# Optimization experiments

Measured on AMD Instinct MI355X. Metric: run time of the kernel, lower is better.

Reference implementation:

```python
import jax, jax.numpy as jnp
import numpy as np

B = 128
N_ATOMS = 4096
NB, NA, NT = 4095, 4094, 4093
MAX_LEN = 5 * NT  # 20465, longest packed column (torsions)
EPS = 1e-8


def setup_inputs() -> dict:
    key = jax.random.key(0)
    ks = jax.random.split(key, 24)
    feats = jnp.zeros((B, MAX_LEN, 9), jnp.float32)
    # col 0: atom type ids
    atoms = jax.random.randint(ks[0], (B, N_ATOMS), 0, 6)
    # col 5: coords, flattened (N_ATOMS, 3)
    coords = jax.random.normal(ks[1], (B, N_ATOMS, 3), jnp.float32) * 5.0
    # col 6: bonds (i, j, type)
    bonds = jnp.stack([
        jax.random.randint(ks[2], (B, NB), 0, N_ATOMS),
        jax.random.randint(ks[3], (B, NB), 0, N_ATOMS),
        jax.random.randint(ks[4], (B, NB), 0, 15)], axis=-1)
    # col 7: angles (i, j, k, type)
    angles = jnp.stack([
        jax.random.randint(ks[5], (B, NA), 0, N_ATOMS),
        jax.random.randint(ks[6], (B, NA), 0, N_ATOMS),
        jax.random.randint(ks[7], (B, NA), 0, N_ATOMS),
        jax.random.randint(ks[8], (B, NA), 0, 13)], axis=-1)
    # col 8: torsions (i, j, k, l, type)
    tors = jnp.stack([
        jax.random.randint(ks[9], (B, NT), 0, N_ATOMS),
        jax.random.randint(ks[10], (B, NT), 0, N_ATOMS),
        jax.random.randint(ks[11], (B, NT), 0, N_ATOMS),
        jax.random.randint(ks[12], (B, NT), 0, N_ATOMS),
        jax.random.randint(ks[13], (B, NT), 0, 25)], axis=-1)
    feats = feats.at[:, :N_ATOMS, 0].set(atoms.astype(jnp.float32))
    feats = feats.at[:, :3 * N_ATOMS, 5].set(coords.reshape(B, -1))
    feats = feats.at[:, :3 * NB, 6].set(bonds.reshape(B, -1).astype(jnp.float32))
    feats = feats.at[:, :4 * NA, 7].set(angles.reshape(B, -1).astype(jnp.float32))
    feats = feats.at[:, :5 * NT, 8].set(tors.reshape(B, -1).astype(jnp.float32))
    lengths = jnp.tile(jnp.array(
        [[N_ATOMS, 0, 0, 0, 0, 3 * N_ATOMS, 3 * NB, 4 * NA, 5 * NT]],
        jnp.int32), (B, 1))
    bond_type = jnp.stack([jnp.ones(15), jax.random.uniform(ks[14], (15,), minval=1.0, maxval=2.0)], -1).astype(jnp.float32)
    angle_type = jnp.stack([jnp.ones(13), jax.random.uniform(ks[15], (13,), minval=1.0, maxval=3.0)], -1).astype(jnp.float32)
    tor_type = jnp.stack([jnp.ones(25), jax.random.uniform(ks[16], (25,), minval=0.0, maxval=3.14)], -1).astype(jnp.float32)
    multiplicity = jax.random.randint(ks[17], (25,), 1, 4)
    opt_pars = jax.random.uniform(ks[18], (47,), minval=0.5, maxval=1.5).astype(jnp.float32)
    return {"features": feats, "lengths": lengths, "bond_type": bond_type,
            "angle_type": angle_type, "tor_type": tor_type,
            "multiplicity": multiplicity, "opt_pars": opt_pars}


def _sample_energy(f, bond_type, angle_type, tor_type, multiplicity, opt_pars):
    coords = f[:3 * N_ATOMS, 5].reshape(-1, 3)                      # [N,3]
    bonds = f[:3 * NB, 6].astype(jnp.int32).reshape(-1, 3)          # [NB,3]
    angles = f[:4 * NA, 7].astype(jnp.int32).reshape(-1, 4)         # [NA,4]
    tors = f[:5 * NT, 8].astype(jnp.int32).reshape(-1, 5)           # [NT,5]

    # bonds: harmonic k*(r - r0)^2
    d = coords[bonds[:, 0]] - coords[bonds[:, 1]]
    r = jnp.sqrt(jnp.sum(d * d, -1) + EPS)
    pb = bond_type[bonds[:, 2]]
    e_bond = opt_pars[0] * jnp.sum(pb[:, 0] * (r - pb[:, 1]) ** 2)

    # angles: harmonic k*(theta - theta0)^2
    v1 = coords[angles[:, 0]] - coords[angles[:, 1]]
    v2 = coords[angles[:, 2]] - coords[angles[:, 1]]
    cosang = jnp.sum(v1 * v2, -1) / (
        jnp.sqrt(jnp.sum(v1 * v1, -1) + EPS) * jnp.sqrt(jnp.sum(v2 * v2, -1) + EPS))
    theta = jnp.arccos(jnp.clip(cosang, -1.0 + 1e-6, 1.0 - 1e-6))
    pa = angle_type[angles[:, 3]]
    e_ang = opt_pars[1] * jnp.sum(pa[:, 0] * (theta - pa[:, 1]) ** 2)

    # torsions: periodic k*(1 + cos(n*phi - delta))
    ci, cj, ck, cl = (coords[tors[:, m]] for m in range(4))
    b1, b2, b3 = cj - ci, ck - cj, cl - ck
    n1 = jnp.cross(b1, b2)
    n2 = jnp.cross(b2, b3)
    b2n = b2 / jnp.sqrt(jnp.sum(b2 * b2, -1, keepdims=True) + EPS)
    m1 = jnp.cross(n1, b2n)
    phi = jnp.arctan2(jnp.sum(m1 * n2, -1), jnp.sum(n1 * n2, -1))
    pt = tor_type[tors[:, 4]]
    n_mult = multiplicity[tors[:, 4]].astype(jnp.float32)
    e_tor = opt_pars[2] * jnp.sum(pt[:, 0] * (1.0 + jnp.cos(n_mult * phi - pt[:, 1])))

    return jnp.stack([e_bond, e_ang, e_tor])


def reference(features, lengths, bond_type, angle_type, tor_type, multiplicity, opt_pars):
    # lengths are uniform across batch (constants above); vmap over batch dim
    return jax.vmap(_sample_energy, in_axes=(0, None, None, None, None, None))(
        features, bond_type, angle_type, tor_type, multiplicity, opt_pars)
```

## Files before the change

kernel.cpp:

```cpp
#include <hip/hip_runtime.h>
#include <math.h>

#define BATCH    128
#define N_ATOMS  4096
#define NB       4095
#define NA       4094
#define NT       4093
#define FSTRIDE  184185
#define ROWS     20465
#define CROWS    12288
#define BROWS    12285
#define AROWS    16376
#define EPSV     1e-8f
#define THREADS  1024
#define WAVES    16
#define TPR      120

typedef float float4a __attribute__((ext_vector_type(4), aligned(4)));

__global__ __launch_bounds__(THREADS, 1) void
local_energy_v11(const float* __restrict__ F,
                 const float* __restrict__ bond_type,
                 const float* __restrict__ angle_type,
                 const float* __restrict__ tor_type,
                 const int*   __restrict__ multiplicity,
                 const float* __restrict__ opt_pars,
                 float*       __restrict__ out)
{
    __shared__ float          scc[CROWS];
    __shared__ unsigned short sbB[BROWS + 1];
    __shared__ unsigned short sbA[AROWS];
    __shared__ unsigned short sbT[ROWS + 1];
    __shared__ float sbt[30], sat[26], stt[50], smu[25];
    __shared__ float sred[WAVES * 2];

    const int b   = blockIdx.x;
    const int x   = b & 7;
    const int g   = b >> 3;
    const int s   = (g & 15) * 8 + x;
    const int p   = g >> 4;
    const int tid = threadIdx.x;
    const int w   = tid >> 6;
    const int l   = tid & 63;
    const size_t sbase = (size_t)s * FSTRIDE;

    if (tid < 30)                      sbt[tid]       = bond_type[tid];
    else if (tid >= 32 && tid < 58)    sat[tid - 32]  = angle_type[tid - 32];
    else if (tid >= 64 && tid < 114)   stt[tid - 64]  = tor_type[tid - 64];
    else if (tid >= 128 && tid < 153)  smu[tid - 128] = (float)multiplicity[tid - 128];

    const int tmax = p ? 137 : 171;
    for (int t = w; t < tmax; t += WAVES) {
        const int R0 = TPR * t + 2 * l;
        const int R1 = R0 + 1;
        float4a v0, v1;
        const bool ok0 = (R0 < ROWS);
        const bool ok1 = (R1 < ROWS);
        if (ok0) v0 = *(const float4a*)(F + sbase + (size_t)9 * R0 + 5);
        if (ok1) v1 = *(const float4a*)(F + sbase + (size_t)9 * R1 + 5);

        if (R1 < CROWS) {
            float2 c2; c2.x = v0.x; c2.y = v1.x;
            *(float2*)(scc + R0) = c2;
        }
        if (p) {
            if (R1 < BROWS) {
                unsigned pk = (unsigned)(unsigned short)(int)v0.y
                            | ((unsigned)(unsigned short)(int)v1.y << 16);
                *(unsigned*)(sbB + R0) = pk;
            } else if (R0 < BROWS) {
                sbB[R0] = (unsigned short)(int)v0.y;
            }
            if (R1 < AROWS) {
                unsigned pk = (unsigned)(unsigned short)(int)v0.z
                            | ((unsigned)(unsigned short)(int)v1.z << 16);
                *(unsigned*)(sbA + R0) = pk;
            }
        } else {
            if (ok1) {
                unsigned pk = (unsigned)(unsigned short)(int)v0.w
                            | ((unsigned)(unsigned short)(int)v1.w << 16);
                *(unsigned*)(sbT + R0) = pk;
            } else if (ok0) {
                sbT[R0] = (unsigned short)(int)v0.w;
            }
        }
    }
    __syncthreads();

    float eA = 0.f, eB = 0.f;
    if (p) {
        for (int i = tid; i < NB; i += THREADS) {
            const int a0 = sbB[3 * i + 0];
            const int a1 = sbB[3 * i + 1];
            const int bt = sbB[3 * i + 2];
            const float dx = scc[3 * a0 + 0] - scc[3 * a1 + 0];
            const float dy = scc[3 * a0 + 1] - scc[3 * a1 + 1];
            const float dz = scc[3 * a0 + 2] - scc[3 * a1 + 2];
            const float r  = sqrtf(dx * dx + dy * dy + dz * dz + EPSV);
            const float t0 = r - sbt[bt * 2 + 1];
            eA += sbt[bt * 2 + 0] * t0 * t0;
        }
        for (int i = tid; i < NA; i += THREADS) {
            const int a0 = sbA[4 * i + 0];
            const int a1 = sbA[4 * i + 1];
            const int a2 = sbA[4 * i + 2];
            const int at = sbA[4 * i + 3];
            const float v1x = scc[3 * a0 + 0] - scc[3 * a1 + 0];
            const float v1y = scc[3 * a0 + 1] - scc[3 * a1 + 1];
            const float v1z = scc[3 * a0 + 2] - scc[3 * a1 + 2];
            const float v2x = scc[3 * a2 + 0] - scc[3 * a1 + 0];
            const float v2y = scc[3 * a2 + 1] - scc[3 * a1 + 1];
            const float v2z = scc[3 * a2 + 2] - scc[3 * a1 + 2];
            const float d12 = v1x * v2x + v1y * v2y + v1z * v2z;
            const float n1  = sqrtf(v1x * v1x + v1y * v1y + v1z * v1z + EPSV);
            const float n2  = sqrtf(v2x * v2x + v2y * v2y + v2z * v2z + EPSV);
            float cosang = d12 / (n1 * n2);
            cosang = fminf(fmaxf(cosang, -1.0f + 1e-6f), 1.0f - 1e-6f);
            const float t0 = acosf(cosang) - sat[at * 2 + 1];
            eB += sat[at * 2 + 0] * t0 * t0;
        }
    } else {
        for (int i = tid; i < NT; i += THREADS) {
            const int ai = sbT[5 * i + 0];
            const int aj = sbT[5 * i + 1];
            const int ak = sbT[5 * i + 2];
            const int al = sbT[5 * i + 3];
            const int tt = sbT[5 * i + 4];
            const float b1x = scc[3*aj+0] - scc[3*ai+0];
            const float b1y = scc[3*aj+1] - scc[3*ai+1];
            const float b1z = scc[3*aj+2] - scc[3*ai+2];
            const float b2x = scc[3*ak+0] - scc[3*aj+0];
            const float b2y = scc[3*ak+1] - scc[3*aj+1];
            const float b2z = scc[3*ak+2] - scc[3*aj+2];
            const float b3x = scc[3*al+0] - scc[3*ak+0];
            const float b3y = scc[3*al+1] - scc[3*ak+1];
            const float b3z = scc[3*al+2] - scc[3*ak+2];
            const float n1x = b1y*b2z - b1z*b2y;
            const float n1y = b1z*b2x - b1x*b2z;
            const float n1z = b1x*b2y - b1y*b2x;
            const float n2x = b2y*b3z - b2z*b3y;
            const float n2y = b2z*b3x - b2x*b3z;
            const float n2z = b2x*b3y - b2y*b3x;
            const float inv = 1.0f / sqrtf(b2x*b2x + b2y*b2y + b2z*b2z + EPSV);
            const float bnx = b2x * inv, bny = b2y * inv, bnz = b2z * inv;
            const float m1x = n1y*bnz - n1z*bny;
            const float m1y = n1z*bnx - n1x*bnz;
            const float m1z = n1x*bny - n1y*bnx;
            const float phi = atan2f(m1x*n2x + m1y*n2y + m1z*n2z,
                                     n1x*n2x + n1y*n2y + n1z*n2z);
            eA += stt[tt * 2 + 0] * (1.0f + cosf(smu[tt] * phi - stt[tt * 2 + 1]));
        }
    }

    for (int off = 32; off > 0; off >>= 1) {
        eA += __shfl_down(eA, off);
        eB += __shfl_down(eB, off);
    }
    if (l == 0) {
        sred[w * 2 + 0] = eA;
        sred[w * 2 + 1] = eB;
    }
    __syncthreads();
    if (tid == 0) {
        float rA = 0.f, rB = 0.f;
        for (int i = 0; i < WAVES; ++i) { rA += sred[i * 2]; rB += sred[i * 2 + 1]; }
        if (p) {
            out[s * 3 + 0] = opt_pars[0] * rA;
            out[s * 3 + 1] = opt_pars[1] * rB;
        } else {
            out[s * 3 + 2] = opt_pars[2] * rA;
        }
    }
}

extern "C" void kernel_launch(void* const* d_in, const int* in_sizes, int n_in,
                              void* d_out, int out_size, void* d_ws, size_t ws_size,
                              hipStream_t stream) {
    const float* F            = (const float*)d_in[0];
    const float* bond_type    = (const float*)d_in[2];
    const float* angle_type   = (const float*)d_in[3];
    const float* tor_type     = (const float*)d_in[4];
    const int*   multiplicity = (const int*)  d_in[5];
    const float* opt_pars     = (const float*)d_in[6];
    float* out = (float*)d_out;

    local_energy_v11<<<dim3(BATCH * 2), dim3(THREADS), 0, stream>>>(
        F, bond_type, angle_type, tor_type, multiplicity, opt_pars, out);
}
```

Baseline: 154.1 us.

## Merge bond/angle and torsion blocks into one block per sample

Replaces the two-blocks-per-sample split, where one block did bonds and angles and the other did torsions, with a single 1024-thread block per sample that computes all three energies. Each sample's feature rows are then staged into shared memory once instead of twice, removing redundant global reads of the coordinate column. The staging loop is also unrolled by two so each wave issues four vector loads before any shared-memory stores. The trade-off is half as many blocks (128 versus 256) and longer serial work per block, which can leave many compute units idle on a large GPU.

```diff
diff --git a/kernel.cpp b/kernel.cpp
--- a/kernel.cpp
+++ b/kernel.cpp
@@ -15,11 +15,13 @@
 #define THREADS  1024
 #define WAVES    16
 #define TPR      120
+#define NTILES   171
 
 typedef float float4a __attribute__((ext_vector_type(4), aligned(4)));
 
+
 __global__ __launch_bounds__(THREADS, 1) void
-local_energy_v11(const float* __restrict__ F,
+local_energy_v12(const float* __restrict__ F,
                  const float* __restrict__ bond_type,
                  const float* __restrict__ angle_type,
                  const float* __restrict__ tor_type,
@@ -32,13 +34,9 @@
     __shared__ unsigned short sbA[AROWS];
     __shared__ unsigned short sbT[ROWS + 1];
     __shared__ float sbt[30], sat[26], stt[50], smu[25];
-    __shared__ float sred[WAVES * 2];
-
-    const int b   = blockIdx.x;
-    const int x   = b & 7;
-    const int g   = b >> 3;
-    const int s   = (g & 15) * 8 + x;
-    const int p   = g >> 4;
+    __shared__ float sred[WAVES * 3];
+
+    const int s   = blockIdx.x;
     const int tid = threadIdx.x;
     const int w   = tid >> 6;
     const int l   = tid & 63;
@@ -49,128 +47,160 @@
     else if (tid >= 64 && tid < 114)   stt[tid - 64]  = tor_type[tid - 64];
     else if (tid >= 128 && tid < 153)  smu[tid - 128] = (float)multiplicity[tid - 128];
 
-    const int tmax = p ? 137 : 171;
-    for (int t = w; t < tmax; t += WAVES) {
-        const int R0 = TPR * t + 2 * l;
-        const int R1 = R0 + 1;
-        float4a v0, v1;
-        const bool ok0 = (R0 < ROWS);
-        const bool ok1 = (R1 < ROWS);
-        if (ok0) v0 = *(const float4a*)(F + sbase + (size_t)9 * R0 + 5);
-        if (ok1) v1 = *(const float4a*)(F + sbase + (size_t)9 * R1 + 5);
-
-        if (R1 < CROWS) {
-            float2 c2; c2.x = v0.x; c2.y = v1.x;
-            *(float2*)(scc + R0) = c2;
-        }
-        if (p) {
+    for (int t = w; t < NTILES; t += 2 * WAVES) {
+        const int tb  = t + WAVES;
+        const int R0a = TPR * t  + 2 * l;
+        const int R0b = TPR * tb + 2 * l;
+        const bool ok0a = (R0a     < ROWS);
+        const bool ok1a = (R0a + 1 < ROWS);
+        const bool ok0b = (R0b     < ROWS);
+        const bool ok1b = (R0b + 1 < ROWS);
+        const float* pa = F + sbase + (size_t)9 * R0a + 5;
+        const float* pb = F + sbase + (size_t)9 * R0b + 5;
+        float4a v0a, v1a, v0b, v1b;
+        if (ok0a) v0a = *(const float4a*)(pa);
+        if (ok1a) v1a = *(const float4a*)(pa + 9);
+        if (ok0b) v0b = *(const float4a*)(pb);
+        if (ok1b) v1b = *(const float4a*)(pb + 9);
+
+        {
+            const int R0 = R0a, R1 = R0a + 1;
+            if (R1 < CROWS) {
+                float2 c2; c2.x = v0a.x; c2.y = v1a.x;
+                *(float2*)(scc + R0) = c2;
+            }
             if (R1 < BROWS) {
-                unsigned pk = (unsigned)(unsigned short)(int)v0.y
-                            | ((unsigned)(unsigned short)(int)v1.y << 16);
+                unsigned pk = (unsigned)(unsigned short)(int)v0a.y
+                            | ((unsigned)(unsigned short)(int)v1a.y << 16);
                 *(unsigned*)(sbB + R0) = pk;
             } else if (R0 < BROWS) {
-                sbB[R0] = (unsigned short)(int)v0.y;
+                sbB[R0] = (unsigned short)(int)v0a.y;
             }
             if (R1 < AROWS) {
-                unsigned pk = (unsigned)(unsigned short)(int)v0.z
-                            | ((unsigned)(unsigned short)(int)v1.z << 16);
+                unsigned pk = (unsigned)(unsigned short)(int)v0a.z
+                            | ((unsigned)(unsigned short)(int)v1a.z << 16);
                 *(unsigned*)(sbA + R0) = pk;
             }
-        } else {
-            if (ok1) {
-                unsigned pk = (unsigned)(unsigned short)(int)v0.w
-                            | ((unsigned)(unsigned short)(int)v1.w << 16);
+            if (ok1a) {
+                unsigned pk = (unsigned)(unsigned short)(int)v0a.w
+                            | ((unsigned)(unsigned short)(int)v1a.w << 16);
                 *(unsigned*)(sbT + R0) = pk;
-            } else if (ok0) {
-                sbT[R0] = (unsigned short)(int)v0.w;
+            } else if (ok0a) {
+                sbT[R0] = (unsigned short)(int)v0a.w;
             }
         }
+        {
+            const int R0 = R0b, R1 = R0b + 1;
+            if (R1 < CROWS) {
+                float2 c2; c2.x = v0b.x; c2.y = v1b.x;
+                *(float2*)(scc + R0) = c2;
+            }
+            if (R1 < BROWS) {
+                unsigned pk = (unsigned)(unsigned short)(int)v0b.y
+                            | ((unsigned)(unsigned short)(int)v1b.y << 16);
+                *(unsigned*)(sbB + R0) = pk;
+            } else if (R0 < BROWS) {
+                sbB[R0] = (unsigned short)(int)v0b.y;
+            }
+            if (R1 < AROWS) {
+                unsigned pk = (unsigned)(unsigned short)(int)v0b.z
+                            | ((unsigned)(unsigned short)(int)v1b.z << 16);
+                *(unsigned*)(sbA + R0) = pk;
+            }
+            if (ok1b) {
+                unsigned pk = (unsigned)(unsigned short)(int)v0b.w
+                            | ((unsigned)(unsigned short)(int)v1b.w << 16);
+                *(unsigned*)(sbT + R0) = pk;
+            } else if (ok0b) {
+                sbT[R0] = (unsigned short)(int)v0b.w;
+            }
+        }
     }
     __syncthreads();
 
-    float eA = 0.f, eB = 0.f;
-    if (p) {
-        for (int i = tid; i < NB; i += THREADS) {
-            const int a0 = sbB[3 * i + 0];
-            const int a1 = sbB[3 * i + 1];
-            const int bt = sbB[3 * i + 2];
-            const float dx = scc[3 * a0 + 0] - scc[3 * a1 + 0];
-            const float dy = scc[3 * a0 + 1] - scc[3 * a1 + 1];
-            const float dz = scc[3 * a0 + 2] - scc[3 * a1 + 2];
-            const float r  = sqrtf(dx * dx + dy * dy + dz * dz + EPSV);
-            const float t0 = r - sbt[bt * 2 + 1];
-            eA += sbt[bt * 2 + 0] * t0 * t0;
-        }
-        for (int i = tid; i < NA; i += THREADS) {
-            const int a0 = sbA[4 * i + 0];
-            const int a1 = sbA[4 * i + 1];
-            const int a2 = sbA[4 * i + 2];
-            const int at = sbA[4 * i + 3];
-            const float v1x = scc[3 * a0 + 0] - scc[3 * a1 + 0];
-            const float v1y = scc[3 * a0 + 1] - scc[3 * a1 + 1];
-            const float v1z = scc[3 * a0 + 2] - scc[3 * a1 + 2];
-            const float v2x = scc[3 * a2 + 0] - scc[3 * a1 + 0];
-            const float v2y = scc[3 * a2 + 1] - scc[3 * a1 + 1];
-            const float v2z = scc[3 * a2 + 2] - scc[3 * a1 + 2];
-            const float d12 = v1x * v2x + v1y * v2y + v1z * v2z;
-            const float n1  = sqrtf(v1x * v1x + v1y * v1y + v1z * v1z + EPSV);
-            const float n2  = sqrtf(v2x * v2x + v2y * v2y + v2z * v2z + EPSV);
-            float cosang = d12 / (n1 * n2);
-            cosang = fminf(fmaxf(cosang, -1.0f + 1e-6f), 1.0f - 1e-6f);
-            const float t0 = acosf(cosang) - sat[at * 2 + 1];
-            eB += sat[at * 2 + 0] * t0 * t0;
-        }
-    } else {
-        for (int i = tid; i < NT; i += THREADS) {
-            const int ai = sbT[5 * i + 0];
-            const int aj = sbT[5 * i + 1];
-            const int ak = sbT[5 * i + 2];
-            const int al = sbT[5 * i + 3];
-            const int tt = sbT[5 * i + 4];
-            const float b1x = scc[3*aj+0] - scc[3*ai+0];
-            const float b1y = scc[3*aj+1] - scc[3*ai+1];
-            const float b1z = scc[3*aj+2] - scc[3*ai+2];
-            const float b2x = scc[3*ak+0] - scc[3*aj+0];
-            const float b2y = scc[3*ak+1] - scc[3*aj+1];
-            const float b2z = scc[3*ak+2] - scc[3*aj+2];
-            const float b3x = scc[3*al+0] - scc[3*ak+0];
-            const float b3y = scc[3*al+1] - scc[3*ak+1];
-            const float b3z = scc[3*al+2] - scc[3*ak+2];
-            const float n1x = b1y*b2z - b1z*b2y;
-            const float n1y = b1z*b2x - b1x*b2z;
-            const float n1z = b1x*b2y - b1y*b2x;
-            const float n2x = b2y*b3z - b2z*b3y;
-            const float n2y = b2z*b3x - b2x*b3z;
-            const float n2z = b2x*b3y - b2y*b3x;
-            const float inv = 1.0f / sqrtf(b2x*b2x + b2y*b2y + b2z*b2z + EPSV);
-            const float bnx = b2x * inv, bny = b2y * inv, bnz = b2z * inv;
-            const float m1x = n1y*bnz - n1z*bny;
-            const float m1y = n1z*bnx - n1x*bnz;
-            const float m1z = n1x*bny - n1y*bnx;
-            const float phi = atan2f(m1x*n2x + m1y*n2y + m1z*n2z,
-                                     n1x*n2x + n1y*n2y + n1z*n2z);
-            eA += stt[tt * 2 + 0] * (1.0f + cosf(smu[tt] * phi - stt[tt * 2 + 1]));
-        }
+    float eB = 0.f, eG = 0.f, eT = 0.f;
+    for (int i = tid; i < NB; i += THREADS) {
+        const int a0 = sbB[3 * i + 0];
+        const int a1 = sbB[3 * i + 1];
+        const int bt = sbB[3 * i + 2];
+        const float dx = scc[3 * a0 + 0] - scc[3 * a1 + 0];
+        const float dy = scc[3 * a0 + 1] - scc[3 * a1 + 1];
+        const float dz = scc[3 * a0 + 2] - scc[3 * a1 + 2];
+        const float r  = sqrtf(dx * dx + dy * dy + dz * dz + EPSV);
+        const float t0 = r - sbt[bt * 2 + 1];
+        eB += sbt[bt * 2 + 0] * t0 * t0;
+    }
+    for (int i = tid; i < NA; i += THREADS) {
+        const int a0 = sbA[4 * i + 0];
+        const int a1 = sbA[4 * i + 1];
+        const int a2 = sbA[4 * i + 2];
+        const int at = sbA[4 * i + 3];
+        const float v1x = scc[3 * a0 + 0] - scc[3 * a1 + 0];
+        const float v1y = scc[3 * a0 + 1] - scc[3 * a1 + 1];
+        const float v1z = scc[3 * a0 + 2] - scc[3 * a1 + 2];
+        const float v2x = scc[3 * a2 + 0] - scc[3 * a1 + 0];
+        const float v2y = scc[3 * a2 + 1] - scc[3 * a1 + 1];
+        const float v2z = scc[3 * a2 + 2] - scc[3 * a1 + 2];
+        const float d12 = v1x * v2x + v1y * v2y + v1z * v2z;
+        const float n1  = sqrtf(v1x * v1x + v1y * v1y + v1z * v1z + EPSV);
+        const float n2  = sqrtf(v2x * v2x + v2y * v2y + v2z * v2z + EPSV);
+        float cosang = d12 / (n1 * n2);
+        cosang = fminf(fmaxf(cosang, -1.0f + 1e-6f), 1.0f - 1e-6f);
+        const float t0 = acosf(cosang) - sat[at * 2 + 1];
+        eG += sat[at * 2 + 0] * t0 * t0;
+    }
+    for (int i = tid; i < NT; i += THREADS) {
+        const int ai = sbT[5 * i + 0];
+        const int aj = sbT[5 * i + 1];
+        const int ak = sbT[5 * i + 2];
+        const int al = sbT[5 * i + 3];
+        const int tt = sbT[5 * i + 4];
+        const float b1x = scc[3*aj+0] - scc[3*ai+0];
+        const float b1y = scc[3*aj+1] - scc[3*ai+1];
+        const float b1z = scc[3*aj+2] - scc[3*ai+2];
+        const float b2x = scc[3*ak+0] - scc[3*aj+0];
+        const float b2y = scc[3*ak+1] - scc[3*aj+1];
+        const float b2z = scc[3*ak+2] - scc[3*aj+2];
+        const float b3x = scc[3*al+0] - scc[3*ak+0];
+        const float b3y = scc[3*al+1] - scc[3*ak+1];
+        const float b3z = scc[3*al+2] - scc[3*ak+2];
+        const float n1x = b1y*b2z - b1z*b2y;
+        const float n1y = b1z*b2x - b1x*b2z;
+        const float n1z = b1x*b2y - b1y*b2x;
+        const float n2x = b2y*b3z - b2z*b3y;
+        const float n2y = b2z*b3x - b2x*b3z;
+        const float n2z = b2x*b3y - b2y*b3x;
+        const float inv = 1.0f / sqrtf(b2x*b2x + b2y*b2y + b2z*b2z + EPSV);
+        const float bnx = b2x * inv, bny = b2y * inv, bnz = b2z * inv;
+        const float m1x = n1y*bnz - n1z*bny;
+        const float m1y = n1z*bnx - n1x*bnz;
+        const float m1z = n1x*bny - n1y*bnx;
+        const float phi = atan2f(m1x*n2x + m1y*n2y + m1z*n2z,
+                                 n1x*n2x + n1y*n2y + n1z*n2z);
+        eT += stt[tt * 2 + 0] * (1.0f + cosf(smu[tt] * phi - stt[tt * 2 + 1]));
     }
 
     for (int off = 32; off > 0; off >>= 1) {
-        eA += __shfl_down(eA, off);
         eB += __shfl_down(eB, off);
+        eG += __shfl_down(eG, off);
+        eT += __shfl_down(eT, off);
     }
     if (l == 0) {
-        sred[w * 2 + 0] = eA;
-        sred[w * 2 + 1] = eB;
+        sred[w * 3 + 0] = eB;
+        sred[w * 3 + 1] = eG;
+        sred[w * 3 + 2] = eT;
     }
     __syncthreads();
     if (tid == 0) {
-        float rA = 0.f, rB = 0.f;
-        for (int i = 0; i < WAVES; ++i) { rA += sred[i * 2]; rB += sred[i * 2 + 1]; }
-        if (p) {
-            out[s * 3 + 0] = opt_pars[0] * rA;
-            out[s * 3 + 1] = opt_pars[1] * rB;
-        } else {
-            out[s * 3 + 2] = opt_pars[2] * rA;
+        float rB = 0.f, rG = 0.f, rT = 0.f;
+        for (int i = 0; i < WAVES; ++i) {
+            rB += sred[i * 3 + 0];
+            rG += sred[i * 3 + 1];
+            rT += sred[i * 3 + 2];
         }
+        out[s * 3 + 0] = opt_pars[0] * rB;
+        out[s * 3 + 1] = opt_pars[1] * rG;
+        out[s * 3 + 2] = opt_pars[2] * rT;
     }
 }
 
@@ -185,6 +215,6 @@
     const float* opt_pars     = (const float*)d_in[6];
     float* out = (float*)d_out;
 
-    local_energy_v11<<<dim3(BATCH * 2), dim3(THREADS), 0, stream>>>(
+    local_energy_v12<<<dim3(BATCH), dim3(THREADS), 0, stream>>>(
         F, bond_type, angle_type, tor_type, multiplicity, opt_pars, out);
 }
```

After: 166.2 us. 1.08x slower.

## Stage feature rows through double-buffered LDS chunks with coalesced float4 loads

Applied to the files above, without the earlier changes.

Replaces the strided per-row float4 gathers (stride 9 floats) with fully contiguous float4 loads of 736-row chunks into a double-buffered LDS staging area, then extracts columns 5-8 from LDS. Loads of the next chunk are issued into registers before extracting the current one, overlapping global latency with the LDS work. Index arrays are unioned to fit the staging buffers in LDS. The cost is more barriers and more LDS traffic, and each block now reads the full row width, including unused columns, for its range of rows.

```diff
diff --git a/kernel.cpp b/kernel.cpp
--- a/kernel.cpp
+++ b/kernel.cpp
@@ -14,12 +14,19 @@
 #define EPSV     1e-8f
 #define THREADS  1024
 #define WAVES    16
-#define TPR      120
+
+#define CH_ROWS  736
+#define SCHUNK   6624
+#define NF4      1656
+#define NCH_P0   28
+#define NCH_P1   23
 
 typedef float float4a __attribute__((ext_vector_type(4), aligned(4)));
+typedef float float4w __attribute__((ext_vector_type(4), aligned(16)));
+
 
 __global__ __launch_bounds__(THREADS, 1) void
-local_energy_v11(const float* __restrict__ F,
+local_energy_v13(const float* __restrict__ F,
                  const float* __restrict__ bond_type,
                  const float* __restrict__ angle_type,
                  const float* __restrict__ tor_type,
@@ -27,10 +34,13 @@
                  const float* __restrict__ opt_pars,
                  float*       __restrict__ out)
 {
-    __shared__ float          scc[CROWS];
-    __shared__ unsigned short sbB[BROWS + 1];
-    __shared__ unsigned short sbA[AROWS];
-    __shared__ unsigned short sbT[ROWS + 1];
+    __shared__ float scc[CROWS];
+    __shared__ __align__(16) float stg[2][SCHUNK];
+    __shared__ union IdxU {
+        struct { unsigned short bB[BROWS + 1];
+                 unsigned short bA[AROWS]; } q;
+        unsigned short bT[ROWS + 1];
+    } u;
     __shared__ float sbt[30], sat[26], stt[50], smu[25];
     __shared__ float sred[WAVES * 2];
 
@@ -42,58 +52,84 @@
     const int tid = threadIdx.x;
     const int w   = tid >> 6;
     const int l   = tid & 63;
-    const size_t sbase = (size_t)s * FSTRIDE;
+    const float* Fb = F + (size_t)s * FSTRIDE;
 
     if (tid < 30)                      sbt[tid]       = bond_type[tid];
     else if (tid >= 32 && tid < 58)    sat[tid - 32]  = angle_type[tid - 32];
     else if (tid >= 64 && tid < 114)   stt[tid - 64]  = tor_type[tid - 64];
     else if (tid >= 128 && tid < 153)  smu[tid - 128] = (float)multiplicity[tid - 128];
 
-    const int tmax = p ? 137 : 171;
-    for (int t = w; t < tmax; t += WAVES) {
-        const int R0 = TPR * t + 2 * l;
-        const int R1 = R0 + 1;
-        float4a v0, v1;
-        const bool ok0 = (R0 < ROWS);
-        const bool ok1 = (R1 < ROWS);
-        if (ok0) v0 = *(const float4a*)(F + sbase + (size_t)9 * R0 + 5);
-        if (ok1) v1 = *(const float4a*)(F + sbase + (size_t)9 * R1 + 5);
-
-        if (R1 < CROWS) {
-            float2 c2; c2.x = v0.x; c2.y = v1.x;
-            *(float2*)(scc + R0) = c2;
-        }
-        if (p) {
-            if (R1 < BROWS) {
-                unsigned pk = (unsigned)(unsigned short)(int)v0.y
-                            | ((unsigned)(unsigned short)(int)v1.y << 16);
-                *(unsigned*)(sbB + R0) = pk;
-            } else if (R0 < BROWS) {
-                sbB[R0] = (unsigned short)(int)v0.y;
-            }
-            if (R1 < AROWS) {
-                unsigned pk = (unsigned)(unsigned short)(int)v0.z
-                            | ((unsigned)(unsigned short)(int)v1.z << 16);
-                *(unsigned*)(sbA + R0) = pk;
-            }
-        } else {
-            if (ok1) {
-                unsigned pk = (unsigned)(unsigned short)(int)v0.w
-                            | ((unsigned)(unsigned short)(int)v1.w << 16);
-                *(unsigned*)(sbT + R0) = pk;
-            } else if (ok0) {
-                sbT[R0] = (unsigned short)(int)v0.w;
-            }
-        }
-    }
-    __syncthreads();
+    const int NCH    = p ? NCH_P1 : NCH_P0;
+    const int rowLim = p ? AROWS  : ROWS;
+
+#define LOADC(c, r) do {                                                      \
+        const int _gf0 = (c) * SCHUNK + 4 * tid;                              \
+        if (_gf0 + 4 <= FSTRIDE) r##a = *(const float4a*)(Fb + _gf0);         \
+        if (tid < (NF4 - 1024) && _gf0 + 4096 + 4 <= FSTRIDE)                 \
+            r##b = *(const float4a*)(Fb + _gf0 + 4096);                       \
+        if (!p && (c) == NCH_P0 - 1 && tid == 1023) r##t = Fb[FSTRIDE - 1];   \
+    } while (0)
+
+#define WRITEC(c, buf, r) do {                                                \
+        const int _gf0 = (c) * SCHUNK + 4 * tid;                              \
+        if (_gf0 + 4 <= FSTRIDE) *(float4w*)&stg[buf][4 * tid] = r##a;        \
+        if (tid < (NF4 - 1024) && _gf0 + 4096 + 4 <= FSTRIDE)                 \
+            *(float4w*)&stg[buf][4 * tid + 4096] = r##b;                      \
+        if (!p && (c) == NCH_P0 - 1 && tid == 1023) stg[buf][5336] = r##t;    \
+    } while (0)
+
+#define EXTRACT(c, buf) do {                                                  \
+        if (tid < CH_ROWS) {                                                  \
+            const int _R = (c) * CH_ROWS + tid;                               \
+            if (_R < rowLim) {                                                \
+                const float* _sp = &stg[buf][9 * tid + 5];                    \
+                const float _v5 = _sp[0], _v6 = _sp[1];                       \
+                const float _v7 = _sp[2], _v8 = _sp[3];                       \
+                if (_R < CROWS) scc[_R] = _v5;                                \
+                if (p) {                                                      \
+                    if (_R < BROWS) u.q.bB[_R] = (unsigned short)(int)_v6;    \
+                    u.q.bA[_R] = (unsigned short)(int)_v7;                    \
+                } else {                                                      \
+                    u.bT[_R] = (unsigned short)(int)_v8;                      \
+                }                                                             \
+            }                                                                 \
+        }                                                                     \
+    } while (0)
+
+#define SYNC() do {                                                           \
+        __builtin_amdgcn_sched_barrier(0);                                    \
+        asm volatile("s_waitcnt lgkmcnt(0)");                                 \
+        __builtin_amdgcn_s_barrier();                                         \
+        __builtin_amdgcn_sched_barrier(0);                                    \
+    } while (0)
+
+    float4a rAa, rAb, rBa, rBb;
+    float rAt = 0.f, rBt = 0.f;
+    (void)rAt; (void)rBt;
+
+    LOADC(0, rA);
+    WRITEC(0, 0, rA);
+    LOADC(1, rB);
+    SYNC();
+
+    for (int c = 0; c < NCH; c += 2) {
+        if (c + 2 < NCH) LOADC(c + 2, rA);
+        EXTRACT(c, 0);
+        if (c + 1 < NCH) WRITEC(c + 1, 1, rB);
+        SYNC();
+        if (c + 1 >= NCH) break;
+        if (c + 3 < NCH) LOADC(c + 3, rB);
+        EXTRACT(c + 1, 1);
+        if (c + 2 < NCH) WRITEC(c + 2, 0, rA);
+        SYNC();
+    }
 
     float eA = 0.f, eB = 0.f;
     if (p) {
         for (int i = tid; i < NB; i += THREADS) {
-            const int a0 = sbB[3 * i + 0];
-            const int a1 = sbB[3 * i + 1];
-            const int bt = sbB[3 * i + 2];
+            const int a0 = u.q.bB[3 * i + 0];
+            const int a1 = u.q.bB[3 * i + 1];
+            const int bt = u.q.bB[3 * i + 2];
             const float dx = scc[3 * a0 + 0] - scc[3 * a1 + 0];
             const float dy = scc[3 * a0 + 1] - scc[3 * a1 + 1];
             const float dz = scc[3 * a0 + 2] - scc[3 * a1 + 2];
@@ -102,10 +138,10 @@
             eA += sbt[bt * 2 + 0] * t0 * t0;
         }
         for (int i = tid; i < NA; i += THREADS) {
-            const int a0 = sbA[4 * i + 0];
-            const int a1 = sbA[4 * i + 1];
-            const int a2 = sbA[4 * i + 2];
-            const int at = sbA[4 * i + 3];
+            const int a0 = u.q.bA[4 * i + 0];
+            const int a1 = u.q.bA[4 * i + 1];
+            const int a2 = u.q.bA[4 * i + 2];
+            const int at = u.q.bA[4 * i + 3];
             const float v1x = scc[3 * a0 + 0] - scc[3 * a1 + 0];
             const float v1y = scc[3 * a0 + 1] - scc[3 * a1 + 1];
             const float v1z = scc[3 * a0 + 2] - scc[3 * a1 + 2];
@@ -122,11 +158,11 @@
         }
     } else {
         for (int i = tid; i < NT; i += THREADS) {
-            const int ai = sbT[5 * i + 0];
-            const int aj = sbT[5 * i + 1];
-            const int ak = sbT[5 * i + 2];
-            const int al = sbT[5 * i + 3];
-            const int tt = sbT[5 * i + 4];
+            const int ai = u.bT[5 * i + 0];
+            const int aj = u.bT[5 * i + 1];
+            const int ak = u.bT[5 * i + 2];
+            const int al = u.bT[5 * i + 3];
+            const int tt = u.bT[5 * i + 4];
             const float b1x = scc[3*aj+0] - scc[3*ai+0];
             const float b1y = scc[3*aj+1] - scc[3*ai+1];
             const float b1z = scc[3*aj+2] - scc[3*ai+2];
@@ -161,7 +197,7 @@
         sred[w * 2 + 0] = eA;
         sred[w * 2 + 1] = eB;
     }
-    __syncthreads();
+    SYNC();
     if (tid == 0) {
         float rA = 0.f, rB = 0.f;
         for (int i = 0; i < WAVES; ++i) { rA += sred[i * 2]; rB += sred[i * 2 + 1]; }
@@ -172,6 +208,10 @@
             out[s * 3 + 2] = opt_pars[2] * rA;
         }
     }
+#undef LOADC
+#undef WRITEC
+#undef EXTRACT
+#undef SYNC
 }
 
 extern "C" void kernel_launch(void* const* d_in, const int* in_sizes, int n_in,
@@ -185,6 +225,6 @@
     const float* opt_pars     = (const float*)d_in[6];
     float* out = (float*)d_out;
 
-    local_energy_v11<<<dim3(BATCH * 2), dim3(THREADS), 0, stream>>>(
+    local_energy_v13<<<dim3(BATCH * 2), dim3(THREADS), 0, stream>>>(
         F, bond_type, angle_type, tor_type, multiplicity, opt_pars, out);
 }
```

Result: slower. 163.6 us (+6.2%).

## Split into compaction kernel to workspace and energy kernel reading compact indices

Applied to the files above, without the earlier changes.

Adds a first kernel that reads each sample's strided feature columns once, splitting every sample across two blocks, and writes coords plus 16-bit packed indices into a compact workspace. A second kernel loads the compact data into shared memory and computes the bond/angle or torsion energies. Previously both per-sample blocks re-read the strided 9-column rows (coords read twice). The split adds a kernel launch, a workspace round trip, and a fallback to the old kernel when no workspace is provided.

```diff
diff --git a/kernel.cpp b/kernel.cpp
--- a/kernel.cpp
+++ b/kernel.cpp
@@ -16,7 +16,237 @@
 #define WAVES    16
 #define TPR      120
 
+#define HROWS    10232
+#define K1TILES  86
+#define WS_BOFF  49152
+#define WS_AOFF  73724
+#define WS_TOFF  106476
+#define WS_SLOT  147456
+#define WS_NEED  ((size_t)WS_SLOT * BATCH)
+
 typedef float float4a __attribute__((ext_vector_type(4), aligned(4)));
+
+
+__global__ __launch_bounds__(THREADS, 1) void
+compact_k1(const float* __restrict__ F, unsigned char* __restrict__ ws)
+{
+    __shared__ __align__(16) float          lc[HROWS];
+    __shared__ __align__(16) unsigned short lb[HROWS + 2];
+    __shared__ __align__(16) unsigned short la[HROWS];
+    __shared__ __align__(16) unsigned short lt[HROWS + 2];
+
+    const int b      = blockIdx.x;
+    const int s      = b >> 1;
+    const int h      = b & 1;
+    const int tid    = threadIdx.x;
+    const int w      = tid >> 6;
+    const int l      = tid & 63;
+    const int base   = h * HROWS;
+    const int rcount = HROWS + h;
+    const int limC   = max(0, min(CROWS - base, rcount));
+    const int limB   = max(0, min(BROWS - base, rcount));
+    const int limA   = max(0, min(AROWS - base, rcount));
+    const int limT   = rcount;
+    const float* Fb  = F + (size_t)s * FSTRIDE;
+
+    for (int t = w; t < K1TILES; t += WAVES) {
+        const int r0 = TPR * t + 2 * l;
+        const int r1 = r0 + 1;
+        float4a v0, v1;
+        if (r0 < rcount) v0 = *(const float4a*)(Fb + (size_t)9 * (base + r0) + 5);
+        if (r1 < rcount) v1 = *(const float4a*)(Fb + (size_t)9 * (base + r1) + 5);
+
+        if (r1 < limC) {
+            float2 c2; c2.x = v0.x; c2.y = v1.x;
+            *(float2*)(lc + r0) = c2;
+        } else if (r0 < limC) {
+            lc[r0] = v0.x;
+        }
+        if (r1 < limB) {
+            unsigned pk = (unsigned)(unsigned short)(int)v0.y
+                        | ((unsigned)(unsigned short)(int)v1.y << 16);
+            *(unsigned*)(lb + r0) = pk;
+        } else if (r0 < limB) {
+            lb[r0] = (unsigned short)(int)v0.y;
+        }
+        if (r1 < limA) {
+            unsigned pk = (unsigned)(unsigned short)(int)v0.z
+                        | ((unsigned)(unsigned short)(int)v1.z << 16);
+            *(unsigned*)(la + r0) = pk;
+        } else if (r0 < limA) {
+            la[r0] = (unsigned short)(int)v0.z;
+        }
+        if (r1 < limT) {
+            unsigned pk = (unsigned)(unsigned short)(int)v0.w
+                        | ((unsigned)(unsigned short)(int)v1.w << 16);
+            *(unsigned*)(lt + r0) = pk;
+        } else if (r0 < limT) {
+            lt[r0] = (unsigned short)(int)v0.w;
+        }
+    }
+    __syncthreads();
+
+    unsigned char* wsS = ws + (size_t)s * WS_SLOT;
+    {
+        const unsigned* src = (const unsigned*)lc;
+        unsigned*       dst = (unsigned*)wsS + base;
+        for (int i = tid; i < limC; i += THREADS) dst[i] = src[i];
+    }
+    {
+        const unsigned* src = (const unsigned*)lb;
+        unsigned*       dst = (unsigned*)(wsS + WS_BOFF) + (base >> 1);
+        const int n = (limB * 2 + 3) >> 2;
+        for (int i = tid; i < n; i += THREADS) dst[i] = src[i];
+    }
+    {
+        const unsigned* src = (const unsigned*)la;
+        unsigned*       dst = (unsigned*)(wsS + WS_AOFF) + (base >> 1);
+        const int n = (limA * 2 + 3) >> 2;
+        for (int i = tid; i < n; i += THREADS) dst[i] = src[i];
+    }
+    {
+        const unsigned* src = (const unsigned*)lt;
+        unsigned*       dst = (unsigned*)(wsS + WS_TOFF) + (base >> 1);
+        const int n = (limT * 2 + 3) >> 2;
+        for (int i = tid; i < n; i += THREADS) dst[i] = src[i];
+    }
+}
+
+__global__ __launch_bounds__(THREADS, 1) void
+energy_k2(const unsigned char* __restrict__ ws,
+          const float* __restrict__ bond_type,
+          const float* __restrict__ angle_type,
+          const float* __restrict__ tor_type,
+          const int*   __restrict__ multiplicity,
+          const float* __restrict__ opt_pars,
+          float*       __restrict__ out)
+{
+    __shared__ float scc[CROWS];
+    __shared__ union IdxU {
+        struct { unsigned short bB[BROWS + 1];
+                 unsigned short bA[AROWS]; } q;
+        unsigned short bT[ROWS + 1];
+    } u;
+    __shared__ float sbt[30], sat[26], stt[50], smu[25];
+    __shared__ float sred[WAVES * 2];
+
+    const int b   = blockIdx.x;
+    const int s   = b & 127;
+    const int p   = b >> 7;
+    const int tid = threadIdx.x;
+    const int w   = tid >> 6;
+    const int l   = tid & 63;
+
+    if (tid < 30)                      sbt[tid]       = bond_type[tid];
+    else if (tid >= 32 && tid < 58)    sat[tid - 32]  = angle_type[tid - 32];
+    else if (tid >= 64 && tid < 114)   stt[tid - 64]  = tor_type[tid - 64];
+    else if (tid >= 128 && tid < 153)  smu[tid - 128] = (float)multiplicity[tid - 128];
+
+    const unsigned char* wsS = ws + (size_t)s * WS_SLOT;
+    {
+        const unsigned* src = (const unsigned*)wsS;
+        unsigned*       dst = (unsigned*)scc;
+        for (int i = tid; i < 12288; i += THREADS) dst[i] = src[i];
+    }
+    if (p) {
+        const unsigned* srcB = (const unsigned*)(wsS + WS_BOFF);
+        unsigned*       dstB = (unsigned*)u.q.bB;
+        for (int i = tid; i < 6143; i += THREADS) dstB[i] = srcB[i];
+        const unsigned* srcA = (const unsigned*)(wsS + WS_AOFF);
+        unsigned*       dstA = (unsigned*)u.q.bA;
+        for (int i = tid; i < 8188; i += THREADS) dstA[i] = srcA[i];
+    } else {
+        const unsigned* srcT = (const unsigned*)(wsS + WS_TOFF);
+        unsigned*       dstT = (unsigned*)u.bT;
+        for (int i = tid; i < 10233; i += THREADS) dstT[i] = srcT[i];
+    }
+    __syncthreads();
+
+    float eA = 0.f, eB = 0.f;
+    if (p) {
+        for (int i = tid; i < NB; i += THREADS) {
+            const int a0 = u.q.bB[3 * i + 0];
+            const int a1 = u.q.bB[3 * i + 1];
+            const int bt = u.q.bB[3 * i + 2];
+            const float dx = scc[3 * a0 + 0] - scc[3 * a1 + 0];
+            const float dy = scc[3 * a0 + 1] - scc[3 * a1 + 1];
+            const float dz = scc[3 * a0 + 2] - scc[3 * a1 + 2];
+            const float r  = sqrtf(dx * dx + dy * dy + dz * dz + EPSV);
+            const float t0 = r - sbt[bt * 2 + 1];
+            eA += sbt[bt * 2 + 0] * t0 * t0;
+        }
+        for (int i = tid; i < NA; i += THREADS) {
+            const int a0 = u.q.bA[4 * i + 0];
+            const int a1 = u.q.bA[4 * i + 1];
+            const int a2 = u.q.bA[4 * i + 2];
+            const int at = u.q.bA[4 * i + 3];
+            const float v1x = scc[3 * a0 + 0] - scc[3 * a1 + 0];
+            const float v1y = scc[3 * a0 + 1] - scc[3 * a1 + 1];
+            const float v1z = scc[3 * a0 + 2] - scc[3 * a1 + 2];
+            const float v2x = scc[3 * a2 + 0] - scc[3 * a1 + 0];
+            const float v2y = scc[3 * a2 + 1] - scc[3 * a1 + 1];
+            const float v2z = scc[3 * a2 + 2] - scc[3 * a1 + 2];
+            const float d12 = v1x * v2x + v1y * v2y + v1z * v2z;
+            const float n1  = sqrtf(v1x * v1x + v1y * v1y + v1z * v1z + EPSV);
+            const float n2  = sqrtf(v2x * v2x + v2y * v2y + v2z * v2z + EPSV);
+            float cosang = d12 / (n1 * n2);
+            cosang = fminf(fmaxf(cosang, -1.0f + 1e-6f), 1.0f - 1e-6f);
+            const float t0 = acosf(cosang) - sat[at * 2 + 1];
+            eB += sat[at * 2 + 0] * t0 * t0;
+        }
+    } else {
+        for (int i = tid; i < NT; i += THREADS) {
+            const int ai = u.bT[5 * i + 0];
+            const int aj = u.bT[5 * i + 1];
+            const int ak = u.bT[5 * i + 2];
+            const int al = u.bT[5 * i + 3];
+            const int tt = u.bT[5 * i + 4];
+            const float b1x = scc[3*aj+0] - scc[3*ai+0];
+            const float b1y = scc[3*aj+1] - scc[3*ai+1];
+            const float b1z = scc[3*aj+2] - scc[3*ai+2];
+            const float b2x = scc[3*ak+0] - scc[3*aj+0];
+            const float b2y = scc[3*ak+1] - scc[3*aj+1];
+            const float b2z = scc[3*ak+2] - scc[3*aj+2];
+            const float b3x = scc[3*al+0] - scc[3*ak+0];
+            const float b3y = scc[3*al+1] - scc[3*ak+1];
+            const float b3z = scc[3*al+2] - scc[3*ak+2];
+            const float n1x = b1y*b2z - b1z*b2y;
+            const float n1y = b1z*b2x - b1x*b2z;
+            const float n1z = b1x*b2y - b1y*b2x;
+            const float n2x = b2y*b3z - b2z*b3y;
+            const float n2y = b2z*b3x - b2x*b3z;
+            const float n2z = b2x*b3y - b2y*b3x;
+            const float inv = 1.0f / sqrtf(b2x*b2x + b2y*b2y + b2z*b2z + EPSV);
+            const float bnx = b2x * inv, bny = b2y * inv, bnz = b2z * inv;
+            const float m1x = n1y*bnz - n1z*bny;
+            const float m1y = n1z*bnx - n1x*bnz;
+            const float m1z = n1x*bny - n1y*bnx;
+            const float phi = atan2f(m1x*n2x + m1y*n2y + m1z*n2z,
+                                     n1x*n2x + n1y*n2y + n1z*n2z);
+            eA += stt[tt * 2 + 0] * (1.0f + cosf(smu[tt] * phi - stt[tt * 2 + 1]));
+        }
+    }
+
+    for (int off = 32; off > 0; off >>= 1) {
+        eA += __shfl_down(eA, off);
+        eB += __shfl_down(eB, off);
+    }
+    if (l == 0) {
+        sred[w * 2 + 0] = eA;
+        sred[w * 2 + 1] = eB;
+    }
+    __syncthreads();
+    if (tid == 0) {
+        float rA = 0.f, rB = 0.f;
+        for (int i = 0; i < WAVES; ++i) { rA += sred[i * 2]; rB += sred[i * 2 + 1]; }
+        if (p) {
+            out[s * 3 + 0] = opt_pars[0] * rA;
+            out[s * 3 + 1] = opt_pars[1] * rB;
+        } else {
+            out[s * 3 + 2] = opt_pars[2] * rA;
+        }
+    }
+}
 
 __global__ __launch_bounds__(THREADS, 1) void
 local_energy_v11(const float* __restrict__ F,
@@ -58,7 +288,6 @@
         const bool ok1 = (R1 < ROWS);
         if (ok0) v0 = *(const float4a*)(F + sbase + (size_t)9 * R0 + 5);
         if (ok1) v1 = *(const float4a*)(F + sbase + (size_t)9 * R1 + 5);
-
         if (R1 < CROWS) {
             float2 c2; c2.x = v0.x; c2.y = v1.x;
             *(float2*)(scc + R0) = c2;
@@ -185,6 +414,14 @@
     const float* opt_pars     = (const float*)d_in[6];
     float* out = (float*)d_out;
 
-    local_energy_v11<<<dim3(BATCH * 2), dim3(THREADS), 0, stream>>>(
-        F, bond_type, angle_type, tor_type, multiplicity, opt_pars, out);
+    if (d_ws != nullptr && ws_size >= WS_NEED) {
+        compact_k1<<<dim3(BATCH * 2), dim3(THREADS), 0, stream>>>(
+            F, (unsigned char*)d_ws);
+        energy_k2<<<dim3(BATCH * 2), dim3(THREADS), 0, stream>>>(
+            (const unsigned char*)d_ws, bond_type, angle_type, tor_type,
+            multiplicity, opt_pars, out);
+    } else {
+        local_energy_v11<<<dim3(BATCH * 2), dim3(THREADS), 0, stream>>>(
+            F, bond_type, angle_type, tor_type, multiplicity, opt_pars, out);
+    }
 }
```

New measurement: 168.2 us. 9.2% more time.
